# Optimization experiments

Hardware: AMD Instinct MI355X
Metric: run time of the kernel (lower is better)

The kernel has to match this reference:

```python
import jax, jax.numpy as jnp
import numpy as np
from jax import lax

B, C, H, W = 8, 256, 64, 64
HEADS = 8
STRIDE = 2


def _grouped_conv(x, w, b, stride, groups):
    # x: [B, Cin, H, W]; w: [Cout, Cin/groups, k, k] (OIHW)
    y = lax.conv_general_dilated(x, w, (stride, stride), 'VALID',
                                 dimension_numbers=('NCHW', 'OIHW', 'NCHW'),
                                 feature_group_count=groups)
    return y + b[None, :, None, None]


def _grouped_conv_transpose(x, w, b, stride, groups):
    # Equivalent of torch ConvTranspose2d(kernel=stride, stride=stride, groups=groups)
    # implemented as lhs-dilated conv. w: [Cout, Cin/groups, k, k] (already in conv-equivalent layout).
    k = w.shape[-1]
    pad = k - 1
    y = lax.conv_general_dilated(x, w, (1, 1), [(pad, pad), (pad, pad)],
                                 lhs_dilation=(stride, stride),
                                 dimension_numbers=('NCHW', 'OIHW', 'NCHW'),
                                 feature_group_count=groups)
    return y + b[None, :, None, None]


def setup_inputs() -> dict:
    key = jax.random.key(0)
    ks = jax.random.split(key, 12)
    s = 0.05
    inp = {
        'q': jax.random.normal(ks[0], (B, C, H, W), jnp.float32),
        'k': jax.random.normal(ks[1], (B, C, H, W), jnp.float32),
        'v': jax.random.normal(ks[2], (B, C, H, W), jnp.float32),
        # grouped QKV conv weights: groups=C, out=C*HEADS -> [C*HEADS, 1, s, s]
        'wq': jax.random.normal(ks[3], (C * HEADS, 1, STRIDE, STRIDE), jnp.float32) * s,
        'bq': jax.random.normal(ks[4], (C * HEADS,), jnp.float32) * s,
        'wk': jax.random.normal(ks[5], (C * HEADS, 1, STRIDE, STRIDE), jnp.float32) * s,
        'bk': jax.random.normal(ks[6], (C * HEADS,), jnp.float32) * s,
        'wv': jax.random.normal(ks[7], (C * HEADS, 1, STRIDE, STRIDE), jnp.float32) * s,
        'bv': jax.random.normal(ks[8], (C * HEADS,), jnp.float32) * s,
        # deconv (groups=C, in=C*HEADS, out=C) in conv-equivalent OIHW layout: [C, HEADS, s, s]
        'wo': jax.random.normal(ks[9], (C, HEADS, STRIDE, STRIDE), jnp.float32) * s,
        'bo': jax.random.normal(ks[10], (C,), jnp.float32) * s,
        'gamma': jax.random.normal(ks[11], (1,), jnp.float32),
    }
    return inp


def reference(q, k, v, wq, bq, wk, bk, wv, bv, wo, bo, gamma):
    Bn, Cq, Hq, Wsp = q.shape
    Ckv = k.shape[1]
    # grouped conv projections -> [B, heads, C, L]
    pq = _grouped_conv(q, wq, bq, STRIDE, Cq).reshape(Bn, HEADS, Cq, -1)
    pk = _grouped_conv(k, wk, bk, STRIDE, Ckv).reshape(Bn, HEADS, Ckv, -1)
    pv = _grouped_conv(v, wv, bv, STRIDE, Ckv).reshape(Bn, HEADS, Ckv, -1)
    scale = pq.shape[3] ** (-0.5)
    # channel-wise attention: [B, h, Cq, Ckv]
    attn = jax.nn.softmax(jnp.einsum('bhcl,bhdl->bhcd', pq, pk) * scale, axis=-1)
    out = jnp.einsum('bhcd,bhdl->bhcl', attn, pv)  # [B, h, Cq, L]
    out = out.reshape(Bn, HEADS * Cq, Hq // STRIDE, Wsp // STRIDE)
    out = _grouped_conv_transpose(out, wo, bo, STRIDE, Cq)  # [B, Cq, Hq, Wsp]
    # dropout is identity at inference
    return q + out * gamma
```

## Files before the change

kernel.cpp:

```cpp
#include <hip/hip_runtime.h>
#include <hip/hip_bf16.h>

typedef __bf16 bf16;
typedef __bf16 bf16x4 __attribute__((ext_vector_type(4)));
typedef __bf16 bf16x8 __attribute__((ext_vector_type(8)));
typedef float f32x4 __attribute__((ext_vector_type(4)));

__device__ __forceinline__ void gload16(const void* g, void* l) {
  __builtin_amdgcn_global_load_lds(
      (const __attribute__((address_space(1))) unsigned int*)g,
      (__attribute__((address_space(3))) unsigned int*)l, 16, 0, 0);
}


__global__ __launch_bounds__(256) void proj_kqv(
    const float* __restrict__ kin, const float* __restrict__ qin,
    const float* __restrict__ vin,
    const float* __restrict__ wk, const float* __restrict__ bk,
    const float* __restrict__ wq, const float* __restrict__ bq,
    const float* __restrict__ wv, const float* __restrict__ bv,
    bf16* __restrict__ Pk, bf16* __restrict__ Pq, bf16* __restrict__ Vt) {
  int b = blockIdx.y;
  int x = blockIdx.x;
  int t = threadIdx.x;
  int wave = t >> 6, lane = t & 63;
  __shared__ __attribute__((aligned(16))) char smem[32768];
  if (x < 256) {
    bool isq = x >= 128;
    int g0 = (x & 127)*2;
    const float* in   = isq ? qin : kin;
    const float* w    = isq ? wq : wk;
    const float* bias = isq ? bq : bk;
    bf16* out         = isq ? Pq : Pk;
    int j = (t >> 3) & 7, n = t & 7;
    float4 wv0 = reinterpret_cast<const float4*>(w)[g0*8 + j];
    float  bb0 = bias[g0*8 + j];
    float4 wv1 = reinterpret_cast<const float4*>(w)[g0*8 + 8 + j];
    float  bb1 = bias[g0*8 + 8 + j];
    __builtin_amdgcn_sched_barrier(0);
    const char* s0 = (const char*)(in + ((size_t)b*256 + g0)*4096) + wave*4096 + lane*16;
    char* d0 = smem + wave*4096;
    char* d1 = smem + 16384 + wave*4096;
#pragma unroll
    for (int i = 0; i < 4; i++) gload16(s0 + i*1024, d0 + i*1024);
    __builtin_amdgcn_sched_barrier(0);
#pragma unroll
    for (int i = 0; i < 4; i++) gload16(s0 + 16384 + i*1024, d1 + i*1024);
    __builtin_amdgcn_sched_barrier(0);
    int h = g0 >> 5;
    int bh = b*8 + h;

#define CONVST(bufp, g, wvv, bj) { \
    const float* chf = reinterpret_cast<const float*>(bufp); \
    int c0l = ((g) & 31)*8; \
    _Pragma("unroll") \
    for (int p = 0; p < 4; p++) { \
      int kb = p*4 + wave; \
      int m = kb*2 + (n >> 2); \
      int n0 = (n & 3)*8; \
      float rr0[16], rr1[16]; \
      const float4* R0 = reinterpret_cast<const float4*>(chf + (2*m)*64 + 2*n0); \
      const float4* R1 = reinterpret_cast<const float4*>(chf + (2*m+1)*64 + 2*n0); \
      _Pragma("unroll") \
      for (int u = 0; u < 4; u++) { \
        *reinterpret_cast<float4*>(rr0 + u*4) = R0[u]; \
        *reinterpret_cast<float4*>(rr1 + u*4) = R1[u]; \
      } \
      bf16x8 o; \
      _Pragma("unroll") \
      for (int u = 0; u < 8; u++) \
        o[u] = (bf16)((bj) + (wvv).x*rr0[2*u] + (wvv).y*rr0[2*u+1] + (wvv).z*rr1[2*u] + (wvv).w*rr1[2*u+1]); \
      size_t off = (((size_t)bh*16 + kb)*256 + c0l + j)*64 + (size_t)((n ^ j)*8); \
      *reinterpret_cast<bf16x8*>(out + off) = o; \
    } }

    asm volatile("s_waitcnt vmcnt(4)" ::: "memory");
    __builtin_amdgcn_s_barrier();
    CONVST(smem, g0, wv0, bb0);
    __builtin_amdgcn_sched_barrier(0);
    asm volatile("s_waitcnt vmcnt(4)" ::: "memory");
    __builtin_amdgcn_s_barrier();
    CONVST(smem + 16384, g0 + 1, wv1, bb1);
#undef CONVST
  } else {
    float* ch = reinterpret_cast<float*>(smem);
    int r = x - 256;
    int m = r & 31, h = r >> 5;
    {
      int seg = t >> 2, part = t & 3;
      int gl = seg >> 1, ky = seg & 1;
      const float* src = vin + (((size_t)b*256 + h*32 + gl)*64 + (2*m + ky))*64;
      float* drow = ch + (gl*2 + ky)*67;
#pragma unroll
      for (int i = 0; i < 4; i++) {
        float4 v = reinterpret_cast<const float4*>(src)[part + i*4];
        int x0 = (part + i*4)*4;
        drow[x0]=v.x; drow[x0+1]=v.y; drow[x0+2]=v.z; drow[x0+3]=v.w;
      }
    }
    int cgrp = t & 31, lgr = t >> 5;
    int c0 = cgrp*8;
    float4 wv8[8]; float bb8[8];
#pragma unroll
    for (int u = 0; u < 8; u++) {
      wv8[u] = reinterpret_cast<const float4*>(wv)[h*256 + c0 + u];
      bb8[u] = bv[h*256 + c0 + u];
    }
    __syncthreads();
    const float* r0 = ch + (cgrp*2 + 0)*67;
    const float* r1 = ch + (cgrp*2 + 1)*67;
    int bh = b*8 + h;
    bf16* base = Vt + ((size_t)bh*4 + (c0 >> 6))*1024*64;
    int colx = (c0 & 63) ^ (lgr << 3);
#pragma unroll
    for (int p = 0; p < 4; p++) {
      int n = p*8 + lgr;
      int l = m*32 + n;
      float c00 = r0[2*n], c01 = r0[2*n+1], c10 = r1[2*n], c11 = r1[2*n+1];
      bf16x8 o;
#pragma unroll
      for (int u = 0; u < 8; u++)
        o[u] = (bf16)(bb8[u] + wv8[u].x*c00 + wv8[u].y*c01 + wv8[u].z*c10 + wv8[u].w*c11);
      *reinterpret_cast<bf16x8*>(base + (size_t)l*64 + colx) = o;
    }
  }
}

__global__ __launch_bounds__(256, 2) void attn_qk(
    const bf16* __restrict__ Pq, const bf16* __restrict__ Pk,
    bf16* __restrict__ Pattn) {
  int raw = blockIdx.x;
  int idx = raw >> 3;
  int bh = (raw & 7)*8 + (idx >> 2);
  int cs = idx & 3;
  int t = threadIdx.x, wave = t >> 6, lane = t & 63, lg = lane >> 4, lr = lane & 15;
  __shared__ __attribute__((aligned(16))) char smem[81920];
  bf16* Kb0 = reinterpret_cast<bf16*>(smem);
  bf16* Kb1 = reinterpret_cast<bf16*>(smem + 32768);
  bf16* Qb0 = reinterpret_cast<bf16*>(smem + 65536);
  bf16* Qb1 = reinterpret_cast<bf16*>(smem + 73728);
  float (*red)[64] = reinterpret_cast<float (*)[64]>(smem + 65536);
  bf16* Pst = reinterpret_cast<bf16*>(smem);
  const char* Kbase = (const char*)Pk + (size_t)bh*524288 + wave*8192 + lane*16;
  const char* Qbase = (const char*)Pq + (size_t)bh*524288 + (size_t)cs*8192 + wave*2048 + lane*16;
  char* Kd0 = (char*)Kb0 + wave*8192;  char* Kd1 = (char*)Kb1 + wave*8192;
  char* Qd0 = (char*)Qb0 + wave*2048;  char* Qd1 = (char*)Qb1 + wave*2048;

#define STAGE(kb, K_, Q_) { \
    const char* kc = Kbase + (size_t)(kb)*32768; \
    _Pragma("unroll") \
    for (int i_ = 0; i_ < 8; i_++) gload16(kc + i_*1024, (K_) + i_*1024); \
    const char* qc = Qbase + (size_t)(kb)*32768; \
    gload16(qc, (Q_)); gload16(qc + 1024, (Q_) + 1024); }

  f32x4 acc[4][4];
#pragma unroll
  for (int i = 0; i < 4; i++)
#pragma unroll
    for (int j = 0; j < 4; j++) { f32x4 z = {0.f,0.f,0.f,0.f}; acc[i][j] = z; }

  STAGE(0, Kd0, Qd0);
#pragma unroll
  for (int kb = 0; kb < 16; kb++) {
    if (kb < 15) {
      if (kb & 1) { STAGE(kb+1, Kd0, Qd0); } else { STAGE(kb+1, Kd1, Qd1); }
      asm volatile("s_waitcnt vmcnt(10)" ::: "memory");
    } else {
      asm volatile("s_waitcnt vmcnt(0)" ::: "memory");
    }
    __builtin_amdgcn_s_barrier();
    __builtin_amdgcn_sched_barrier(0);
    const bf16* Kc = (kb & 1) ? Kb1 : Kb0;
    const bf16* Qc = (kb & 1) ? Qb1 : Qb0;
#pragma unroll
    for (int ks = 0; ks < 2; ks++) {
      int colx = (ks*32 + lg*8) ^ ((lr & 7) << 3);
      bf16x8 a[4];
#pragma unroll
      for (int mi = 0; mi < 4; mi++)
        a[mi] = *reinterpret_cast<const bf16x8*>(Qc + (mi*16 + lr)*64 + colx);
#pragma unroll
      for (int ni = 0; ni < 4; ni++) {
        bf16x8 bv2 = *reinterpret_cast<const bf16x8*>(Kc + (wave*64 + ni*16 + lr)*64 + colx);
#pragma unroll
        for (int mi = 0; mi < 4; mi++)
          acc[mi][ni] = __builtin_amdgcn_mfma_f32_16x16x32_bf16(a[mi], bv2, acc[mi][ni], 0, 0, 0);
      }
    }
    __builtin_amdgcn_s_barrier();
    __builtin_amdgcn_sched_barrier(0);
  }
#undef STAGE
  const float scale = 0.03125f;
  float sums[4][4];
#pragma unroll
  for (int mi = 0; mi < 4; mi++)
#pragma unroll
    for (int r = 0; r < 4; r++) {
      float mx = fmaxf(fmaxf(acc[mi][0][r], acc[mi][1][r]), fmaxf(acc[mi][2][r], acc[mi][3][r]));
#pragma unroll
      for (int off = 1; off < 16; off <<= 1) mx = fmaxf(mx, __shfl_xor(mx, off, 64));
      red[wave][mi*16 + lg*4 + r] = mx;
    }
  __syncthreads();
#pragma unroll
  for (int mi = 0; mi < 4; mi++)
#pragma unroll
    for (int r = 0; r < 4; r++) {
      int clr = mi*16 + lg*4 + r;
      float mx = fmaxf(fmaxf(red[0][clr], red[1][clr]), fmaxf(red[2][clr], red[3][clr]));
      float s = 0.f;
#pragma unroll
      for (int ni = 0; ni < 4; ni++) {
        float p = __expf(scale*(acc[mi][ni][r] - mx));
        acc[mi][ni][r] = p; s += p;
      }
#pragma unroll
      for (int off = 1; off < 16; off <<= 1) s += __shfl_xor(s, off, 64);
      sums[mi][r] = s;
    }
  __syncthreads();
#pragma unroll
  for (int mi = 0; mi < 4; mi++)
#pragma unroll
    for (int r = 0; r < 4; r++) red[wave][mi*16 + lg*4 + r] = sums[mi][r];
  __syncthreads();
#pragma unroll
  for (int mi = 0; mi < 4; mi++)
#pragma unroll
    for (int r = 0; r < 4; r++) {
      int clr = mi*16 + lg*4 + r;
      float iv = 1.f/(red[0][clr] + red[1][clr] + red[2][clr] + red[3][clr]);
#pragma unroll
      for (int ni = 0; ni < 4; ni++) {
        int dl = ni*16 + lr;
        Pst[wave*4096 + clr*64 + (dl ^ ((clr & 7) << 3))] = (bf16)(acc[mi][ni][r]*iv);
      }
    }
  __syncthreads();
  const uint4* ls = reinterpret_cast<const uint4*>(Pst);
#pragma unroll
  for (int i = 0; i < 8; i++) {
    int f = i*256 + t;
    int kb = f >> 9, rem = f & 511;
    char* dst = (char*)Pattn + ((size_t)(bh*4 + kb)*256 + cs*64)*128 + (size_t)rem*16;
    *reinterpret_cast<uint4*>(dst) = ls[f];
  }
}

__global__ __launch_bounds__(256, 4) void pv_deconv(const bf16* __restrict__ Pattn,
    const bf16* __restrict__ Vt, const float* __restrict__ qin,
    const float* __restrict__ wo, const float* __restrict__ bo,
    const float* __restrict__ gamma, float* __restrict__ outp) {
  int raw = blockIdx.x;
  int idx = raw >> 3;
  int pair = (raw & 7)*32 + (idx >> 2);
  int tb = idx & 3;
  int mb = pair & 3, bh = pair >> 2;
  int h = bh & 7, b = bh >> 3;
  int t = threadIdx.x, wave = t >> 6, lane = t & 63, lg = lane >> 4, lr = lane & 15;
  __shared__ __attribute__((aligned(16))) char smem[40960];
  bf16* Pl   = reinterpret_cast<bf16*>(smem);
  bf16* Vl   = reinterpret_cast<bf16*>(smem + 8192);
  bf16* OlT  = reinterpret_cast<bf16*>(smem);
  float* wo_s = reinterpret_cast<float*>(smem + 36864);
  float* bo_s = reinterpret_cast<float*>(smem + 37888);
  const char* Pbase = (const char*)Pattn + ((size_t)bh*4*256 + tb*64)*128;
  const char* Vbase = (const char*)Vt + ((size_t)bh*4*1024 + mb*256)*128;
  f32x4 acc[4][4];
#pragma unroll
  for (int i = 0; i < 4; i++)
#pragma unroll
    for (int j = 0; j < 4; j++) { f32x4 z = {0.f,0.f,0.f,0.f}; acc[i][j] = z; }
  for (int kb = 0; kb < 4; kb++) {
    __syncthreads();
    {
      const char* pc = Pbase + (size_t)kb*32768 + wave*2048 + lane*16;
      char* pl = (char*)Pl + wave*2048;
#pragma unroll
      for (int i = 0; i < 2; i++) gload16(pc + i*1024, pl + i*1024);
      const char* vc = Vbase + (size_t)kb*131072 + wave*8192 + lane*16;
      char* vl = (char*)Vl + wave*8192;
#pragma unroll
      for (int i = 0; i < 8; i++) gload16(vc + i*1024, vl + i*1024);
    }
    __syncthreads();
#pragma unroll
    for (int ks = 0; ks < 2; ks++) {
      int colx = (ks*32 + lg*8) ^ ((lr & 7) << 3);
      bf16x8 a[4];
#pragma unroll
      for (int mi = 0; mi < 4; mi++)
        a[mi] = *reinterpret_cast<const bf16x8*>(Pl + (mi*16 + lr)*64 + colx);
#pragma unroll
      for (int ni = 0; ni < 4; ni++) {
        bf16x8 bv2 = *reinterpret_cast<const bf16x8*>(Vl + (wave*64 + ni*16 + lr)*64 + colx);
#pragma unroll
        for (int mi = 0; mi < 4; mi++)
          acc[mi][ni] = __builtin_amdgcn_mfma_f32_16x16x32_bf16(a[mi], bv2, acc[mi][ni], 0, 0, 0);
      }
    }
  }
  __syncthreads();
#pragma unroll
  for (int mi = 0; mi < 4; mi++)
#pragma unroll
    for (int ni = 0; ni < 4; ni++) {
      int l = wave*64 + ni*16 + lr;
      int cb = mi*16 + lg*4;
      bf16x4 p;
      p[0] = (bf16)acc[mi][ni][0]; p[1] = (bf16)acc[mi][ni][1];
      p[2] = (bf16)acc[mi][ni][2]; p[3] = (bf16)acc[mi][ni][3];
      *reinterpret_cast<bf16x4*>(OlT + l*66 + cb) = p;
    }
  wo_s[t] = wo[((size_t)(h*32 + tb*8 + (t>>5)))*32 + (t & 31)];
  if (t < 8) bo_s[t] = bo[h*32 + tb*8 + t];
  __syncthreads();
  int xq = t & 15, b5 = (t >> 4) & 1, ct = t >> 5;
  float2 wp[8];
#pragma unroll
  for (int j = 0; j < 8; j++)
    wp[j] = *reinterpret_cast<const float2*>(wo_s + ct*32 + j*4 + (1 - b5)*2);
  float bias = bo_s[ct];
  float gm = gamma[0];
  int co = h*32 + tb*8 + ct;
#pragma unroll
  for (int it = 0; it < 8; it++) {
    int y = it*2 + b5;
    int ll0 = it*32 + xq*2;
    bf16x4 o00 = *reinterpret_cast<const bf16x4*>(OlT + ll0*66 + ct*8);
    bf16x4 o01 = *reinterpret_cast<const bf16x4*>(OlT + ll0*66 + ct*8 + 4);
    bf16x4 o10 = *reinterpret_cast<const bf16x4*>(OlT + (ll0+1)*66 + ct*8);
    bf16x4 o11 = *reinterpret_cast<const bf16x4*>(OlT + (ll0+1)*66 + ct*8 + 4);
    float v0 = bias, v1 = bias, v2 = bias, v3 = bias;
#pragma unroll
    for (int j = 0; j < 4; j++) {
      float f0 = (float)o00[j], f1 = (float)o01[j];
      v0 += f0*wp[j].y;   v1 += f0*wp[j].x;
      v0 += f1*wp[4+j].y; v1 += f1*wp[4+j].x;
      float g0 = (float)o10[j], g1 = (float)o11[j];
      v2 += g0*wp[j].y;   v3 += g0*wp[j].x;
      v2 += g1*wp[4+j].y; v3 += g1*wp[4+j].x;
    }
    size_t oi = (((size_t)b*256 + co)*64 + (mb*16 + y))*64 + xq*4;
    float4 qv = *reinterpret_cast<const float4*>(qin + oi);
    float4 ov;
    ov.x = qv.x + gm*v0; ov.y = qv.y + gm*v1;
    ov.z = qv.z + gm*v2; ov.w = qv.w + gm*v3;
    *reinterpret_cast<float4*>(outp + oi) = ov;
  }
}

extern "C" void kernel_launch(void* const* d_in, const int* in_sizes, int n_in,
                              void* d_out, int out_size, void* d_ws, size_t ws_size,
                              hipStream_t stream) {
  const float* q  = (const float*)d_in[0];
  const float* k  = (const float*)d_in[1];
  const float* v  = (const float*)d_in[2];
  const float* wq = (const float*)d_in[3];
  const float* bq = (const float*)d_in[4];
  const float* wk = (const float*)d_in[5];
  const float* bk = (const float*)d_in[6];
  const float* wv = (const float*)d_in[7];
  const float* bv = (const float*)d_in[8];
  const float* wo = (const float*)d_in[9];
  const float* bo = (const float*)d_in[10];
  const float* gamma = (const float*)d_in[11];
  float* out = (float*)d_out;

  char* ws = (char*)d_ws;
  bf16* Pk    = (bf16*)(ws);
  bf16* Vt    = (bf16*)(ws + 33554432);
  bf16* Pattn = (bf16*)(ws + 67108864);
  bf16* Pq    = (bf16*)(ws + 75497472);

  proj_kqv<<<dim3(512, 8), 256, 0, stream>>>(k, q, v, wk, bk, wq, bq, wv, bv, Pk, Pq, Vt);
  attn_qk <<<dim3(256), 256, 0, stream>>>(Pq, Pk, Pattn);
  pv_deconv<<<dim3(1024), 256, 0, stream>>>(Pattn, Vt, q, wo, bo, gamma, out);
}
```

Baseline: 80.52 us.

## Store Q/K projections as FP8 and use FP8 MFMA for QK scores

The Q and K projection outputs are now converted to packed FP8 instead of bf16. The attention-score kernel stages these FP8 tiles through LDS and uses the 16x16x32 FP8 MFMA instead of the bf16 one. This halves the bytes written by the projection kernel and read by the QK kernel, halves the LDS staging footprint, and reduces the number of async loads per stage. The cost is lower-precision attention logits, which may push softmax outputs past the accuracy tolerance.

```diff
diff --git a/kernel.cpp b/kernel.cpp
--- a/kernel.cpp
+++ b/kernel.cpp
@@ -5,6 +5,7 @@
 typedef __bf16 bf16x4 __attribute__((ext_vector_type(4)));
 typedef __bf16 bf16x8 __attribute__((ext_vector_type(8)));
 typedef float f32x4 __attribute__((ext_vector_type(4)));
+typedef long i64;
 
 __device__ __forceinline__ void gload16(const void* g, void* l) {
   __builtin_amdgcn_global_load_lds(
@@ -19,7 +20,7 @@
     const float* __restrict__ wk, const float* __restrict__ bk,
     const float* __restrict__ wq, const float* __restrict__ bq,
     const float* __restrict__ wv, const float* __restrict__ bv,
-    bf16* __restrict__ Pk, bf16* __restrict__ Pq, bf16* __restrict__ Vt) {
+    char* __restrict__ Pk, char* __restrict__ Pq, bf16* __restrict__ Vt) {
   int b = blockIdx.y;
   int x = blockIdx.x;
   int t = threadIdx.x;
@@ -31,7 +32,7 @@
     const float* in   = isq ? qin : kin;
     const float* w    = isq ? wq : wk;
     const float* bias = isq ? bq : bk;
-    bf16* out         = isq ? Pq : Pk;
+    char* out         = isq ? Pq : Pk;
     int j = (t >> 3) & 7, n = t & 7;
     float4 wv0 = reinterpret_cast<const float4*>(w)[g0*8 + j];
     float  bb0 = bias[g0*8 + j];
@@ -66,12 +67,18 @@
         *reinterpret_cast<float4*>(rr0 + u*4) = R0[u]; \
         *reinterpret_cast<float4*>(rr1 + u*4) = R1[u]; \
       } \
-      bf16x8 o; \
+      float ov[8]; \
       _Pragma("unroll") \
       for (int u = 0; u < 8; u++) \
-        o[u] = (bf16)((bj) + (wvv).x*rr0[2*u] + (wvv).y*rr0[2*u+1] + (wvv).z*rr1[2*u] + (wvv).w*rr1[2*u+1]); \
+        ov[u] = (bj) + (wvv).x*rr0[2*u] + (wvv).y*rr0[2*u+1] + (wvv).z*rr1[2*u] + (wvv).w*rr1[2*u+1]; \
+      int w0 = 0, w1 = 0; \
+      w0 = __builtin_amdgcn_cvt_pk_fp8_f32(ov[0], ov[1], w0, false); \
+      w0 = __builtin_amdgcn_cvt_pk_fp8_f32(ov[2], ov[3], w0, true); \
+      w1 = __builtin_amdgcn_cvt_pk_fp8_f32(ov[4], ov[5], w1, false); \
+      w1 = __builtin_amdgcn_cvt_pk_fp8_f32(ov[6], ov[7], w1, true); \
       size_t off = (((size_t)bh*16 + kb)*256 + c0l + j)*64 + (size_t)((n ^ j)*8); \
-      *reinterpret_cast<bf16x8*>(out + off) = o; \
+      int2 st; st.x = w0; st.y = w1; \
+      *reinterpret_cast<int2*>(out + off) = st; \
     } }
 
     asm volatile("s_waitcnt vmcnt(4)" ::: "memory");
@@ -127,31 +134,30 @@
 }
 
 __global__ __launch_bounds__(256, 2) void attn_qk(
-    const bf16* __restrict__ Pq, const bf16* __restrict__ Pk,
+    const char* __restrict__ Pq, const char* __restrict__ Pk,
     bf16* __restrict__ Pattn) {
   int raw = blockIdx.x;
   int idx = raw >> 3;
   int bh = (raw & 7)*8 + (idx >> 2);
   int cs = idx & 3;
   int t = threadIdx.x, wave = t >> 6, lane = t & 63, lg = lane >> 4, lr = lane & 15;
-  __shared__ __attribute__((aligned(16))) char smem[81920];
-  bf16* Kb0 = reinterpret_cast<bf16*>(smem);
-  bf16* Kb1 = reinterpret_cast<bf16*>(smem + 32768);
-  bf16* Qb0 = reinterpret_cast<bf16*>(smem + 65536);
-  bf16* Qb1 = reinterpret_cast<bf16*>(smem + 73728);
-  float (*red)[64] = reinterpret_cast<float (*)[64]>(smem + 65536);
+  __shared__ __attribute__((aligned(16))) char smem[40960];
+  char* Kb0 = smem;
+  char* Kb1 = smem + 16384;
+  char* Qb0 = smem + 32768;
+  char* Qb1 = smem + 36864;
+  float (*red)[64] = reinterpret_cast<float (*)[64]>(smem + 32768);
   bf16* Pst = reinterpret_cast<bf16*>(smem);
-  const char* Kbase = (const char*)Pk + (size_t)bh*524288 + wave*8192 + lane*16;
-  const char* Qbase = (const char*)Pq + (size_t)bh*524288 + (size_t)cs*8192 + wave*2048 + lane*16;
-  char* Kd0 = (char*)Kb0 + wave*8192;  char* Kd1 = (char*)Kb1 + wave*8192;
-  char* Qd0 = (char*)Qb0 + wave*2048;  char* Qd1 = (char*)Qb1 + wave*2048;
+  const char* Kbase = Pk + (size_t)bh*262144 + wave*4096 + lane*16;
+  const char* Qbase = Pq + (size_t)bh*262144 + (size_t)cs*4096 + wave*1024 + lane*16;
+  char* Kd0 = Kb0 + wave*4096;  char* Kd1 = Kb1 + wave*4096;
+  char* Qd0 = Qb0 + wave*1024;  char* Qd1 = Qb1 + wave*1024;
 
 #define STAGE(kb, K_, Q_) { \
-    const char* kc = Kbase + (size_t)(kb)*32768; \
+    const char* kc = Kbase + (size_t)(kb)*16384; \
     _Pragma("unroll") \
-    for (int i_ = 0; i_ < 8; i_++) gload16(kc + i_*1024, (K_) + i_*1024); \
-    const char* qc = Qbase + (size_t)(kb)*32768; \
-    gload16(qc, (Q_)); gload16(qc + 1024, (Q_) + 1024); }
+    for (int i_ = 0; i_ < 4; i_++) gload16(kc + i_*1024, (K_) + i_*1024); \
+    gload16(Qbase + (size_t)(kb)*16384, (Q_)); }
 
   f32x4 acc[4][4];
 #pragma unroll
@@ -164,27 +170,27 @@
   for (int kb = 0; kb < 16; kb++) {
     if (kb < 15) {
       if (kb & 1) { STAGE(kb+1, Kd0, Qd0); } else { STAGE(kb+1, Kd1, Qd1); }
-      asm volatile("s_waitcnt vmcnt(10)" ::: "memory");
+      asm volatile("s_waitcnt vmcnt(5)" ::: "memory");
     } else {
       asm volatile("s_waitcnt vmcnt(0)" ::: "memory");
     }
     __builtin_amdgcn_s_barrier();
     __builtin_amdgcn_sched_barrier(0);
-    const bf16* Kc = (kb & 1) ? Kb1 : Kb0;
-    const bf16* Qc = (kb & 1) ? Qb1 : Qb0;
+    const char* Kc = (kb & 1) ? Kb1 : Kb0;
+    const char* Qc = (kb & 1) ? Qb1 : Qb0;
 #pragma unroll
     for (int ks = 0; ks < 2; ks++) {
       int colx = (ks*32 + lg*8) ^ ((lr & 7) << 3);
-      bf16x8 a[4];
+      i64 a[4];
 #pragma unroll
       for (int mi = 0; mi < 4; mi++)
-        a[mi] = *reinterpret_cast<const bf16x8*>(Qc + (mi*16 + lr)*64 + colx);
+        a[mi] = *reinterpret_cast<const i64*>(Qc + (mi*16 + lr)*64 + colx);
 #pragma unroll
       for (int ni = 0; ni < 4; ni++) {
-        bf16x8 bv2 = *reinterpret_cast<const bf16x8*>(Kc + (wave*64 + ni*16 + lr)*64 + colx);
+        i64 bfr = *reinterpret_cast<const i64*>(Kc + (wave*64 + ni*16 + lr)*64 + colx);
 #pragma unroll
         for (int mi = 0; mi < 4; mi++)
-          acc[mi][ni] = __builtin_amdgcn_mfma_f32_16x16x32_bf16(a[mi], bv2, acc[mi][ni], 0, 0, 0);
+          acc[mi][ni] = __builtin_amdgcn_mfma_f32_16x16x32_fp8_fp8(a[mi], bfr, acc[mi][ni], 0, 0, 0);
       }
     }
     __builtin_amdgcn_s_barrier();
@@ -369,10 +375,10 @@
   float* out = (float*)d_out;
 
   char* ws = (char*)d_ws;
-  bf16* Pk    = (bf16*)(ws);
+  char* Pk    = ws;
+  char* Pq    = ws + 16777216;
   bf16* Vt    = (bf16*)(ws + 33554432);
   bf16* Pattn = (bf16*)(ws + 67108864);
-  bf16* Pq    = (bf16*)(ws + 75497472);
 
   proj_kqv<<<dim3(512, 8), 256, 0, stream>>>(k, q, v, wk, bk, wq, bq, wv, bv, Pk, Pq, Vt);
   attn_qk <<<dim3(256), 256, 0, stream>>>(Pq, Pk, Pattn);
```

After: 74.38 us. 7.6% less time.
